# Optimization experiments

Measured on AMD Instinct MI355X. Metric: run time of the kernel, lower is better.

The kernel has to match this reference:

```python
import jax, jax.numpy as jnp
import numpy as np

B, CH, IMG, P = 16, 3, 384, 16
D, HEADS, DH, MLP, DEPTH = 384, 6, 64, 1536, 6
INNER = HEADS * DH
PD = P * P * 5 * CH          # SPT patch dim = 3840
GRID = IMG // P              # 24
NP = GRID * GRID             # 576 patches
SEQ = NP + 1                 # +cls = 577


def layer_norm(x, g, b, eps=1e-5):
    mu = jnp.mean(x, axis=-1, keepdims=True)
    var = jnp.var(x, axis=-1, keepdims=True)
    return (x - mu) * jax.lax.rsqrt(var + eps) * g + b


def spt_shifts(x):
    # F.pad semantics: (left,right,top,bottom) with negative = crop
    s1 = jnp.pad(x, ((0, 0), (0, 0), (0, 0), (1, 0)))[:, :, :, :-1]  # (1,-1,0,0)
    s2 = jnp.pad(x, ((0, 0), (0, 0), (0, 0), (0, 1)))[:, :, :, 1:]   # (-1,1,0,0)
    s3 = jnp.pad(x, ((0, 0), (0, 0), (1, 0), (0, 0)))[:, :, :-1, :]  # (0,0,1,-1)
    s4 = jnp.pad(x, ((0, 0), (0, 0), (0, 1), (0, 0)))[:, :, 1:, :]   # (0,0,-1,1)
    return jnp.concatenate([x, s1, s2, s3, s4], axis=1)  # [b, 5c, H, W]


def patchify(x):
    # 'b c (h p1) (w p2) -> b (h w) (p1 p2 c)'
    b, c, _, _ = x.shape
    x = x.reshape(b, c, GRID, P, GRID, P)
    x = x.transpose(0, 2, 4, 3, 5, 1)  # b h w p1 p2 c
    return x.reshape(b, GRID * GRID, P * P * c)


def setup_inputs():
    key = jax.random.key(0)
    ks = jax.random.split(key, 16)
    img = jax.random.normal(ks[0], (B, CH, IMG, IMG), jnp.float32)
    spt_g = jnp.ones((PD,), jnp.float32)
    spt_b = jnp.zeros((PD,), jnp.float32)
    spt_w = jax.random.normal(ks[1], (PD, D), jnp.float32) * (1.0 / np.sqrt(PD))
    spt_bias = jnp.zeros((D,), jnp.float32)
    pos = jax.random.normal(ks[2], (1, SEQ, D), jnp.float32) * 0.02
    cls = jax.random.normal(ks[3], (1, 1, D), jnp.float32) * 0.02
    attn_g = jnp.ones((DEPTH, D), jnp.float32)
    attn_b = jnp.zeros((DEPTH, D), jnp.float32)
    temp = jnp.full((DEPTH,), np.log(DH ** -0.5), jnp.float32)
    wqkv = jax.random.normal(ks[4], (DEPTH, D, 3 * INNER), jnp.float32) * 0.02
    wout = jax.random.normal(ks[5], (DEPTH, INNER, D), jnp.float32) * 0.02
    bout = jnp.zeros((DEPTH, D), jnp.float32)
    ff_g = jnp.ones((DEPTH, D), jnp.float32)
    ff_b = jnp.zeros((DEPTH, D), jnp.float32)
    w1 = jax.random.normal(ks[6], (DEPTH, D, MLP), jnp.float32) * 0.02
    b1 = jnp.zeros((DEPTH, MLP), jnp.float32)
    w2 = jax.random.normal(ks[7], (DEPTH, MLP, D), jnp.float32) * 0.02
    b2 = jnp.zeros((DEPTH, D), jnp.float32)
    return {"img": img, "spt_g": spt_g, "spt_b": spt_b, "spt_w": spt_w,
            "spt_bias": spt_bias, "pos": pos, "cls": cls, "attn_g": attn_g,
            "attn_b": attn_b, "temp": temp, "wqkv": wqkv, "wout": wout,
            "bout": bout, "ff_g": ff_g, "ff_b": ff_b, "w1": w1, "b1": b1,
            "w2": w2, "b2": b2}


def vit_forward(img, spt_g, spt_b, spt_w, spt_bias, pos, cls, attn_g, attn_b,
                temp, wqkv, wout, bout, ff_g, ff_b, w1, b1, w2, b2):
    # SPT patch embedding
    x = patchify(spt_shifts(img))                      # [b, NP, PD]
    x = layer_norm(x, spt_g, spt_b) @ spt_w + spt_bias  # [b, NP, D]
    b = x.shape[0]
    cls_tok = jnp.broadcast_to(cls, (b, 1, D))
    x = jnp.concatenate([cls_tok, x], axis=1) + pos[:, :SEQ]

    eye = jnp.eye(SEQ, dtype=bool)
    neg = -jnp.finfo(x.dtype).max

    def block(x, p):
        ag, ab, t, wq, wo, bo, fg, fb, W1, B1, W2, B2 = p
        h = layer_norm(x, ag, ab)
        qkv = h @ wq                                   # [b, n, 3*inner]
        q, k, v = jnp.split(qkv, 3, axis=-1)
        q = q.reshape(b, SEQ, HEADS, DH).transpose(0, 2, 1, 3)
        k = k.reshape(b, SEQ, HEADS, DH).transpose(0, 2, 1, 3)
        v = v.reshape(b, SEQ, HEADS, DH).transpose(0, 2, 1, 3)
        dots = jnp.einsum('bhid,bhjd->bhij', q, k) * jnp.exp(t)
        dots = jnp.where(eye, neg, dots)               # diagonal mask (LSA)
        attn = jax.nn.softmax(dots, axis=-1)
        out = jnp.einsum('bhij,bhjd->bhid', attn, v)
        out = out.transpose(0, 2, 1, 3).reshape(b, SEQ, INNER)
        x = out @ wo + bo + x
        h = layer_norm(x, fg, fb)
        x = jax.nn.gelu(h @ W1 + B1, approximate=False) @ W2 + B2 + x
        return x, None

    params = (attn_g, attn_b, temp, wqkv, wout, bout, ff_g, ff_b, w1, b1, w2, b2)
    x, _ = jax.lax.scan(block, x, params)
    return x


def reference(img, spt_g, spt_b, spt_w, spt_bias, pos, cls, attn_g, attn_b,
              temp, wqkv, wout, bout, ff_g, ff_b, w1, b1, w2, b2):
    return vit_forward(img, spt_g, spt_b, spt_w, spt_bias, pos, cls, attn_g,
                       attn_b, temp, wqkv, wout, bout, ff_g, ff_b, w1, b1,
                       w2, b2)
```

## Files before the change

kernel.cpp:

```cpp
#include <hip/hip_runtime.h>

typedef unsigned short ushort_t;
typedef __bf16 bf16x8 __attribute__((ext_vector_type(8)));
typedef float f32x4 __attribute__((ext_vector_type(4)));

#define SEQ_ 577
#define D_ 384
#define NTOK (16 * 577)

enum { M_QKV = 0, M_OUT, M_MLP1, M_MLP2 };

__device__ inline float b2f(ushort_t u) {
    unsigned int x = ((unsigned int)u) << 16;
    float f; __builtin_memcpy(&f, &x, 4); return f;
}
__device__ inline ushort_t f2b(float f) {
    unsigned int x; __builtin_memcpy(&x, &f, 4);
    x = x + 0x7fffu + ((x >> 16) & 1u);
    return (ushort_t)(x >> 16);
}

__device__ void transpose_tile(const float* __restrict__ src,
                               ushort_t* __restrict__ dst,
                               int ldn, int ldk, int k0, int n0)
{
    __shared__ float t[64][65];
    const int tid = threadIdx.x;
    const int c = tid & 63, rr = tid >> 6;
#pragma unroll
    for (int i = 0; i < 16; i++) {
        int kl = rr + i * 4;
        t[kl][c] = src[(size_t)(k0 + kl) * ldn + n0 + c];
    }
    __syncthreads();
#pragma unroll
    for (int i = 0; i < 16; i++) {
        int nl = rr + i * 4;
        dst[(size_t)(n0 + nl) * ldk + k0 + c] = f2b(t[c][nl]);
    }
}

__global__ __launch_bounds__(256) void prep_all_kernel(
    const float* __restrict__ wqkv, const float* __restrict__ wout,
    const float* __restrict__ w1, const float* __restrict__ w2,
    const float* __restrict__ spt_w,
    ushort_t* __restrict__ W6, ushort_t* __restrict__ spt_wt)
{
    int id = blockIdx.x;
    if (id >= 2592) {
        int r2 = id - 2592;
        int kt = r2 % 60, nt = r2 / 60;
        transpose_tile(spt_w, spt_wt, 384, 3840, kt * 64, nt * 64);
        return;
    }
    int l = id / 432;
    int r = id - l * 432;
    ushort_t* qkv_t  = W6 + (size_t)l * 1769472;
    ushort_t* wout_t = qkv_t + 442368;
    ushort_t* w1_t   = wout_t + 147456;
    ushort_t* w2_t   = w1_t + 589824;
    const float* wq = wqkv + (size_t)l * 442368;
    const float* wo = wout + (size_t)l * 147456;
    const float* W1 = w1 + (size_t)l * 589824;
    const float* W2 = w2 + (size_t)l * 589824;
    if (r < 108) {
        int kt = r / 18, nt = r % 18;
        transpose_tile(wq, qkv_t, 1152, 384, kt * 64, nt * 64);
    } else if (r < 144) {
        r -= 108; int kt = r / 6, nt = r % 6;
        transpose_tile(wo, wout_t, 384, 384, kt * 64, nt * 64);
    } else if (r < 288) {
        r -= 144; int kt = r / 24, nt = r % 24;
        transpose_tile(W1, w1_t, 1536, 384, kt * 64, nt * 64);
    } else {
        r -= 288; int kt = r / 6, nt = r % 6;
        transpose_tile(W2, w2_t, 384, 1536, kt * 64, nt * 64);
    }
}

template <int MODE, int NK>
__global__ __launch_bounds__(256) void gemm12864(
    const ushort_t* __restrict__ A, const ushort_t* __restrict__ Bt,
    ushort_t* __restrict__ Co, const float* __restrict__ bias,
    int M, int ldc)
{
    const int K = NK * 32;
    __shared__ __align__(16) ushort_t As[2][128][40];
    __shared__ __align__(16) ushort_t Bs[2][64][40];

    const int gx = gridDim.x;
    const int nwg = gx * gridDim.y;
    const int f = blockIdx.y * gx + blockIdx.x;
    const int q = nwg >> 3, rr_ = nwg & 7;
    const int xcd = f & 7, ii = f >> 3;
    const int swz = (xcd < rr_ ? xcd * (q + 1) : rr_ * (q + 1) + (xcd - rr_) * q) + ii;
    const int bx = swz % gx, by = swz / gx;

    const int tid = threadIdx.x;
    const int rowBase = by * 128;
    const int colBase = bx * 64;
    const int lr = tid >> 2, lk = (tid & 3) * 8;
    const int wv = tid >> 6, lane = tid & 63;
    const int wm = (wv >> 1) * 64, wn = (wv & 1) * 32;
    const int m16 = lane & 15, q4 = lane >> 4, kb = q4 * 8;

    const ushort_t* pa0 = A + (size_t)(rowBase + lr) * K + lk;
    const ushort_t* pa1 = pa0 + (size_t)64 * K;
    const ushort_t* pb  = Bt + (size_t)(colBase + lr) * K + lk;

    f32x4 acc[4][2];
#pragma unroll
    for (int i = 0; i < 4; i++)
#pragma unroll
        for (int j = 0; j < 2; j++) acc[i][j] = (f32x4){0.f, 0.f, 0.f, 0.f};

    uint4 Ua0, Ua1, Ub, Va0, Va1, Vb;
    auto gloadU = [&](int kt) {
        Ua0 = *(const uint4*)(pa0 + kt * 32);
        Ua1 = *(const uint4*)(pa1 + kt * 32);
        Ub  = *(const uint4*)(pb + kt * 32);
    };
    auto gloadV = [&](int kt) {
        Va0 = *(const uint4*)(pa0 + kt * 32);
        Va1 = *(const uint4*)(pa1 + kt * 32);
        Vb  = *(const uint4*)(pb + kt * 32);
    };
    auto swriteU = [&](int buf) {
        *(uint4*)&As[buf][lr][lk] = Ua0;
        *(uint4*)&As[buf][64 + lr][lk] = Ua1;
        *(uint4*)&Bs[buf][lr][lk] = Ub;
    };
    auto swriteV = [&](int buf) {
        *(uint4*)&As[buf][lr][lk] = Va0;
        *(uint4*)&As[buf][64 + lr][lk] = Va1;
        *(uint4*)&Bs[buf][lr][lk] = Vb;
    };
    auto compute = [&](int buf) {
        bf16x8 af[4];
#pragma unroll
        for (int mt = 0; mt < 4; mt++)
            af[mt] = *(const bf16x8*)&As[buf][wm + mt * 16 + m16][kb];
        bf16x8 b0 = *(const bf16x8*)&Bs[buf][wn + m16][kb];
        bf16x8 b1 = *(const bf16x8*)&Bs[buf][wn + 16 + m16][kb];
#pragma unroll
        for (int mt = 0; mt < 4; mt++) {
            acc[mt][0] = __builtin_amdgcn_mfma_f32_16x16x32_bf16(af[mt], b0, acc[mt][0], 0, 0, 0);
            acc[mt][1] = __builtin_amdgcn_mfma_f32_16x16x32_bf16(af[mt], b1, acc[mt][1], 0, 0, 0);
        }
    };

    gloadU(0);
    swriteU(0);
    gloadU(1);
    gloadV(2);
    __syncthreads();

#pragma unroll
    for (int kt = 0; kt < NK; kt += 2) {
        swriteU(1);
        if (kt + 3 < NK) gloadU(kt + 3);
        compute(0);
        __syncthreads();
        if (kt + 2 < NK) {
            swriteV(0);
            if (kt + 4 < NK) gloadV(kt + 4);
        }
        compute(1);
        __syncthreads();
    }

#pragma unroll
    for (int mt = 0; mt < 4; mt++)
#pragma unroll
        for (int nt = 0; nt < 2; nt++) {
            int col = colBase + wn + nt * 16 + m16;
#pragma unroll
            for (int r = 0; r < 4; r++) {
                int row = rowBase + wm + mt * 16 + q4 * 4 + r;
                if (row >= M) continue;
                float v = acc[mt][nt][r];
                if (MODE == M_QKV) {
                    Co[(size_t)row * ldc + col] = f2b(v);
                } else if (MODE == M_MLP1) {
                    float t = v + bias[col];
                    float u = t * (0.7978845608f + 0.0356774081f * t * t);
                    float e = __builtin_amdgcn_exp2f(2.885390082f * u);
                    float gl = t - t * __builtin_amdgcn_rcpf(e + 1.0f);
                    Co[(size_t)row * ldc + col] = f2b(gl);
                }
            }
        }
}

template <int MODE, int NK>
__global__ __launch_bounds__(256) void gemm64(
    const ushort_t* __restrict__ A, const ushort_t* __restrict__ Bt,
    float* __restrict__ resid, const float* __restrict__ bias,
    int M, int ldc)
{
    const int K = NK * 32;
    __shared__ __align__(16) ushort_t As[2][64][40];
    __shared__ __align__(16) ushort_t Bs[2][64][40];

    const int gx = gridDim.x, gy = gridDim.y;
    const int nwg = gx * gy;
    const int f = blockIdx.y * gx + blockIdx.x;
    const int q = nwg >> 3, rr_ = nwg & 7;
    const int xcd = f & 7, ii = f >> 3;
    const int swz = (xcd < rr_ ? xcd * (q + 1) : rr_ * (q + 1) + (xcd - rr_) * q) + ii;
    const int bx = swz % gx, by = swz / gx;

    const int tid = threadIdx.x;
    const int rowBase = by * 64;
    const int colBase = bx * 64;
    const int lr = tid >> 2, lk = (tid & 3) * 8;
    const int wv = tid >> 6, lane = tid & 63;
    const int wm = (wv >> 1) * 32, wn = (wv & 1) * 32;
    const int m16 = lane & 15, q4 = lane >> 4, kb = q4 * 8;

    const ushort_t* pa = A + (size_t)(rowBase + lr) * K + lk;
    const ushort_t* pb = Bt + (size_t)(colBase + lr) * K + lk;

    f32x4 acc[2][2];
#pragma unroll
    for (int i = 0; i < 2; i++)
#pragma unroll
        for (int j = 0; j < 2; j++) acc[i][j] = (f32x4){0.f, 0.f, 0.f, 0.f};

    uint4 Ua, Ub, Va, Vb;
    auto gloadU = [&](int kt) {
        Ua = *(const uint4*)(pa + kt * 32);
        Ub = *(const uint4*)(pb + kt * 32);
    };
    auto gloadV = [&](int kt) {
        Va = *(const uint4*)(pa + kt * 32);
        Vb = *(const uint4*)(pb + kt * 32);
    };
    auto swriteU = [&](int buf) {
        *(uint4*)&As[buf][lr][lk] = Ua;
        *(uint4*)&Bs[buf][lr][lk] = Ub;
    };
    auto swriteV = [&](int buf) {
        *(uint4*)&As[buf][lr][lk] = Va;
        *(uint4*)&Bs[buf][lr][lk] = Vb;
    };
    auto compute = [&](int buf) {
        bf16x8 a0 = *(const bf16x8*)&As[buf][wm + m16][kb];
        bf16x8 a1 = *(const bf16x8*)&As[buf][wm + 16 + m16][kb];
        bf16x8 b0 = *(const bf16x8*)&Bs[buf][wn + m16][kb];
        bf16x8 b1 = *(const bf16x8*)&Bs[buf][wn + 16 + m16][kb];
        acc[0][0] = __builtin_amdgcn_mfma_f32_16x16x32_bf16(a0, b0, acc[0][0], 0, 0, 0);
        acc[0][1] = __builtin_amdgcn_mfma_f32_16x16x32_bf16(a0, b1, acc[0][1], 0, 0, 0);
        acc[1][0] = __builtin_amdgcn_mfma_f32_16x16x32_bf16(a1, b0, acc[1][0], 0, 0, 0);
        acc[1][1] = __builtin_amdgcn_mfma_f32_16x16x32_bf16(a1, b1, acc[1][1], 0, 0, 0);
    };

    gloadU(0);
    swriteU(0);
    gloadU(1);
    gloadV(2);
    __syncthreads();

#pragma unroll
    for (int kt = 0; kt < NK; kt += 2) {
        swriteU(1);
        if (kt + 3 < NK) gloadU(kt + 3);
        compute(0);
        __syncthreads();
        if (kt + 2 < NK) {
            swriteV(0);
            if (kt + 4 < NK) gloadV(kt + 4);
        }
        compute(1);
        __syncthreads();
    }

#pragma unroll
    for (int im = 0; im < 2; im++)
#pragma unroll
        for (int in = 0; in < 2; in++) {
            int col = colBase + wn + in * 16 + m16;
#pragma unroll
            for (int r = 0; r < 4; r++) {
                int row = rowBase + wm + im * 16 + q4 * 4 + r;
                if (row >= M) continue;
                size_t o = (size_t)row * ldc + col;
                resid[o] = resid[o] + acc[im][in][r] + bias[col];
            }
        }
}

__global__ __launch_bounds__(256) void gemm64_spt_split(
    const ushort_t* __restrict__ A, const ushort_t* __restrict__ Bt,
    float* __restrict__ resid, int rowOff)
{
    __shared__ __align__(16) ushort_t As[2][64][40];
    __shared__ __align__(16) ushort_t Bs[2][64][40];

    const int f = blockIdx.z * 288 + blockIdx.y * 6 + blockIdx.x;
    const int swz = (f & 7) * 144 + (f >> 3);
    const int bz = swz / 288;
    const int rem = swz - bz * 288;
    const int by = rem / 6, bx = rem - by * 6;

    const int K = 3840, nk = 30;
    const int rowBase = by * 64;
    const int colBase = bx * 64;
    const int kbase = bz * 960;

    const int tid = threadIdx.x;
    const int lr = tid >> 2, lk = (tid & 3) * 8;
    const int wv = tid >> 6, lane = tid & 63;
    const int wm = (wv >> 1) * 32, wn = (wv & 1) * 32;
    const int m16 = lane & 15, q4 = lane >> 4, kb = q4 * 8;

    const ushort_t* pa = A + (size_t)(rowBase + lr) * K + kbase + lk;
    const ushort_t* pb = Bt + (size_t)(colBase + lr) * K + kbase + lk;

    f32x4 acc[2][2];
#pragma unroll
    for (int i = 0; i < 2; i++)
#pragma unroll
        for (int j = 0; j < 2; j++) acc[i][j] = (f32x4){0.f, 0.f, 0.f, 0.f};

    uint4 Ua, Ub, Va, Vb;
    auto gloadU = [&](int kt) {
        Ua = *(const uint4*)(pa + kt * 32);
        Ub = *(const uint4*)(pb + kt * 32);
    };
    auto gloadV = [&](int kt) {
        Va = *(const uint4*)(pa + kt * 32);
        Vb = *(const uint4*)(pb + kt * 32);
    };
    auto swriteU = [&](int buf) {
        *(uint4*)&As[buf][lr][lk] = Ua;
        *(uint4*)&Bs[buf][lr][lk] = Ub;
    };
    auto swriteV = [&](int buf) {
        *(uint4*)&As[buf][lr][lk] = Va;
        *(uint4*)&Bs[buf][lr][lk] = Vb;
    };
    auto compute = [&](int buf) {
        bf16x8 a0 = *(const bf16x8*)&As[buf][wm + m16][kb];
        bf16x8 a1 = *(const bf16x8*)&As[buf][wm + 16 + m16][kb];
        bf16x8 b0 = *(const bf16x8*)&Bs[buf][wn + m16][kb];
        bf16x8 b1 = *(const bf16x8*)&Bs[buf][wn + 16 + m16][kb];
        acc[0][0] = __builtin_amdgcn_mfma_f32_16x16x32_bf16(a0, b0, acc[0][0], 0, 0, 0);
        acc[0][1] = __builtin_amdgcn_mfma_f32_16x16x32_bf16(a0, b1, acc[0][1], 0, 0, 0);
        acc[1][0] = __builtin_amdgcn_mfma_f32_16x16x32_bf16(a1, b0, acc[1][0], 0, 0, 0);
        acc[1][1] = __builtin_amdgcn_mfma_f32_16x16x32_bf16(a1, b1, acc[1][1], 0, 0, 0);
    };

    gloadU(0);
    swriteU(0);
    gloadU(1);
    gloadV(2);
    __syncthreads();

    for (int kt = 0; kt < nk; kt += 2) {
        swriteU(1);
        if (kt + 3 < nk) gloadU(kt + 3);
        compute(0);
        __syncthreads();
        if (kt + 2 < nk) {
            swriteV(0);
            if (kt + 4 < nk) gloadV(kt + 4);
        }
        compute(1);
        __syncthreads();
    }

#pragma unroll
    for (int im = 0; im < 2; im++)
#pragma unroll
        for (int in = 0; in < 2; in++) {
            int col = colBase + wn + in * 16 + m16;
#pragma unroll
            for (int r = 0; r < 4; r++) {
                int row = rowBase + wm + im * 16 + q4 * 4 + r;
                int grow = rowOff + row;
                int bb = grow / 576, p = grow - bb * 576;
                size_t o = ((size_t)(bb * SEQ_ + 1 + p)) * D_ + col;
                atomicAdd(&resid[o], acc[im][in][r]);
            }
        }
}

__global__ __launch_bounds__(256) void attn_kernel(
    const ushort_t* __restrict__ qkv, ushort_t* __restrict__ attn,
    const float* __restrict__ temp, int layer)
{
    const int f = blockIdx.y * 10 + blockIdx.x;
    const int swz = (f & 7) * 120 + (f >> 3);
    const int qt = swz % 10;
    const int bh = swz / 10;
    const int b = bh / 6, hd = bh - b * 6;
    const int tid = threadIdx.x;
    const int wv = tid >> 6, lane = tid & 63;
    const int m16 = lane & 15, q4 = lane >> 4;
    const float sc2 = expf(temp[layer]) * 1.44269504f;

    __shared__ __align__(16) ushort_t Ks[64][72];
    __shared__ __align__(16) ushort_t Vt[64][72];
    __shared__ __align__(16) ushort_t Pw[4][16][72];

    const int qrow = qt * 64 + wv * 16 + m16;
    const int qtok = qrow < SEQ_ ? qrow : SEQ_ - 1;
    const ushort_t* qb = qkv + ((size_t)(b * SEQ_ + qtok)) * 1152 + hd * 64;
    bf16x8 qf0 = *(const bf16x8*)(qb + q4 * 8);
    bf16x8 qf1 = *(const bf16x8*)(qb + 32 + q4 * 8);

    f32x4 accO[4];
#pragma unroll
    for (int dt = 0; dt < 4; dt++) accO[dt] = (f32x4){0.f, 0.f, 0.f, 0.f};
    float l_r[4] = {0.f, 0.f, 0.f, 0.f};

    const int skey = tid >> 2;
    const int scol = (tid & 3) * 16;
    const int vp   = tid & 31;
    const int vdh  = (tid >> 5) * 8;

    uint4 kv0, kv1, va, vb2;
    auto loadKV = [&](int kt) {
        int key = kt * 64 + skey;
        int gkey = key < SEQ_ ? key : 0;
        const ushort_t* kb_ = qkv + ((size_t)(b * SEQ_ + gkey)) * 1152 + 384 + hd * 64;
        kv0 = *(const uint4*)(kb_ + scol);
        kv1 = *(const uint4*)(kb_ + scol + 8);
        if (key >= SEQ_) { kv0 = (uint4){0, 0, 0, 0}; kv1 = kv0; }
        int vk0 = kt * 64 + 2 * vp;
        int t0 = vk0 < SEQ_ ? vk0 : 0;
        int t1 = vk0 + 1 < SEQ_ ? vk0 + 1 : 0;
        va  = *(const uint4*)(qkv + ((size_t)(b * SEQ_ + t0)) * 1152 + 768 + hd * 64 + vdh);
        vb2 = *(const uint4*)(qkv + ((size_t)(b * SEQ_ + t1)) * 1152 + 768 + hd * 64 + vdh);
        if (vk0 >= SEQ_) va = (uint4){0, 0, 0, 0};
        if (vk0 + 1 >= SEQ_) vb2 = (uint4){0, 0, 0, 0};
    };

    loadKV(0);

    for (int kt = 0; kt < 10; kt++) {
        __syncthreads();
        *(uint4*)&Ks[skey][scol] = kv0;
        *(uint4*)&Ks[skey][scol + 8] = kv1;
        {
            const ushort_t* e0 = (const ushort_t*)&va;
            const ushort_t* e1 = (const ushort_t*)&vb2;
#pragma unroll
            for (int j = 0; j < 8; j++) {
                unsigned int pack = (unsigned int)e0[j] | ((unsigned int)e1[j] << 16);
                *(unsigned int*)&Vt[vdh + j][2 * vp] = pack;
            }
        }
        __syncthreads();
        if (kt + 1 < 10) loadKV(kt + 1);

        f32x4 s[4];
        __builtin_amdgcn_s_setprio(1);
#pragma unroll
        for (int ct = 0; ct < 4; ct++) {
            bf16x8 b0 = *(const bf16x8*)&Ks[ct * 16 + m16][q4 * 8];
            bf16x8 b1 = *(const bf16x8*)&Ks[ct * 16 + m16][32 + q4 * 8];
            f32x4 z = (f32x4){0.f, 0.f, 0.f, 0.f};
            z = __builtin_amdgcn_mfma_f32_16x16x32_bf16(qf0, b0, z, 0, 0, 0);
            z = __builtin_amdgcn_mfma_f32_16x16x32_bf16(qf1, b1, z, 0, 0, 0);
            s[ct] = z;
        }
        __builtin_amdgcn_s_setprio(0);
        const int rowb = qt * 64 + wv * 16 + q4 * 4;
#pragma unroll
        for (int r = 0; r < 4; r++) {
            float rs = 0.f;
#pragma unroll
            for (int ct = 0; ct < 4; ct++) {
                int col = kt * 64 + ct * 16 + m16;
                float v = s[ct][r] * sc2;
                if (col >= SEQ_ || col == rowb + r) v = -1.0e30f;
                float p = __builtin_amdgcn_exp2f(v);
                s[ct][r] = p;
                rs += p;
            }
            rs += __shfl_xor(rs, 1);
            rs += __shfl_xor(rs, 2);
            rs += __shfl_xor(rs, 4);
            rs += __shfl_xor(rs, 8);
            l_r[r] += rs;
        }
#pragma unroll
        for (int ct = 0; ct < 4; ct++)
#pragma unroll
            for (int r = 0; r < 4; r++)
                Pw[wv][q4 * 4 + r][ct * 16 + m16] = f2b(s[ct][r]);
        bf16x8 pf0 = *(const bf16x8*)&Pw[wv][m16][q4 * 8];
        bf16x8 pf1 = *(const bf16x8*)&Pw[wv][m16][32 + q4 * 8];
        __builtin_amdgcn_s_setprio(1);
#pragma unroll
        for (int dt = 0; dt < 4; dt++) {
            bf16x8 vb0 = *(const bf16x8*)&Vt[dt * 16 + m16][q4 * 8];
            bf16x8 vb1 = *(const bf16x8*)&Vt[dt * 16 + m16][32 + q4 * 8];
            f32x4 o = accO[dt];
            o = __builtin_amdgcn_mfma_f32_16x16x32_bf16(pf0, vb0, o, 0, 0, 0);
            o = __builtin_amdgcn_mfma_f32_16x16x32_bf16(pf1, vb1, o, 0, 0, 0);
            accO[dt] = o;
        }
        __builtin_amdgcn_s_setprio(0);
    }

    const int rowb = qt * 64 + wv * 16 + q4 * 4;
#pragma unroll
    for (int r = 0; r < 4; r++) {
        int grow = rowb + r;
        if (grow >= SEQ_) continue;
        float inv = 1.f / l_r[r];
        ushort_t* op = attn + ((size_t)(b * SEQ_ + grow)) * 384 + hd * 64;
#pragma unroll
        for (int dt = 0; dt < 4; dt++)
            op[dt * 16 + m16] = f2b(accO[dt][r] * inv);
    }
}

__global__ __launch_bounds__(256) void spt_ln_kernel(
    const float* __restrict__ img, const float* __restrict__ gg,
    const float* __restrict__ bb_, ushort_t* __restrict__ Xn, int r0)
{
    int bp = r0 + blockIdx.x;
    int b = bp / 576, p = bp - b * 576;
    int ph = p / 24, pw = p - ph * 24;

    __shared__ float vals[3840];
    __shared__ float red[10];

    const int tid = threadIdx.x;
    const int p1 = tid >> 4, p2 = tid & 15;

    float s = 0.f, sq = 0.f;
#pragma unroll
    for (int plane = 0; plane < 15; plane++) {
        int g5 = plane / 3, ch = plane - g5 * 3;
        int row = ph * 16 + p1, col = pw * 16 + p2;
        if (g5 == 1) col -= 1;
        else if (g5 == 2) col += 1;
        else if (g5 == 3) row -= 1;
        else if (g5 == 4) row += 1;
        float v = 0.f;
        if (row >= 0 && row < 384 && col >= 0 && col < 384)
            v = img[((size_t)(b * 3 + ch) * 384 + row) * 384 + col];
        vals[tid * 15 + plane] = v;
        s += v; sq += v * v;
    }
#pragma unroll
    for (int off = 32; off > 0; off >>= 1) {
        s += __shfl_xor(s, off);
        sq += __shfl_xor(sq, off);
    }
    int wid = tid >> 6;
    if ((tid & 63) == 0) { red[wid] = s; red[4 + wid] = sq; }
    __syncthreads();
    if (tid == 0) {
        float S = red[0] + red[1] + red[2] + red[3];
        float Q = red[4] + red[5] + red[6] + red[7];
        float mean = S / 3840.f;
        float var = Q / 3840.f - mean * mean;
        red[8] = mean;
        red[9] = rsqrtf(var + 1e-5f);
    }
    __syncthreads();
    float mean = red[8], rstd = red[9];
#pragma unroll
    for (int i = 0; i < 15; i++) {
        int k = tid + i * 256;
        float v = (vals[k] - mean) * rstd * gg[k] + bb_[k];
        Xn[(size_t)blockIdx.x * 3840 + k] = f2b(v);
    }
}

__global__ __launch_bounds__(256) void ln_kernel(
    const float* __restrict__ x, const float* __restrict__ g,
    const float* __restrict__ b, ushort_t* __restrict__ h)
{
    int row = blockIdx.x * 4 + (threadIdx.x >> 6);
    int lane = threadIdx.x & 63;
    const float* xr = x + (size_t)row * 384;
    float4 a = *(const float4*)(xr + lane * 4);
    float2 c = *(const float2*)(xr + 256 + lane * 2);
    float s = a.x + a.y + a.z + a.w + c.x + c.y;
    float sq = a.x * a.x + a.y * a.y + a.z * a.z + a.w * a.w
             + c.x * c.x + c.y * c.y;
#pragma unroll
    for (int off = 32; off > 0; off >>= 1) {
        s += __shfl_xor(s, off);
        sq += __shfl_xor(sq, off);
    }
    float mean = s / 384.f;
    float var = sq / 384.f - mean * mean;
    float rstd = rsqrtf(var + 1e-5f);
    float4 gv = *(const float4*)(g + lane * 4);
    float2 gc = *(const float2*)(g + 256 + lane * 2);
    float4 bv = *(const float4*)(b + lane * 4);
    float2 bc = *(const float2*)(b + 256 + lane * 2);
    ushort_t* hr = h + (size_t)row * 384;
    {
        unsigned int lo = (unsigned int)f2b((a.x - mean) * rstd * gv.x + bv.x)
                        | ((unsigned int)f2b((a.y - mean) * rstd * gv.y + bv.y) << 16);
        unsigned int hi = (unsigned int)f2b((a.z - mean) * rstd * gv.z + bv.z)
                        | ((unsigned int)f2b((a.w - mean) * rstd * gv.w + bv.w) << 16);
        *(uint2*)&hr[lane * 4] = make_uint2(lo, hi);
    }
    {
        unsigned int w = (unsigned int)f2b((c.x - mean) * rstd * gc.x + bc.x)
                       | ((unsigned int)f2b((c.y - mean) * rstd * gc.y + bc.y) << 16);
        *(unsigned int*)&hr[256 + lane * 2] = w;
    }
}

__global__ void init_x_kernel(const float* __restrict__ cls,
                              const float* __restrict__ pos,
                              const float* __restrict__ spt_bias,
                              float* __restrict__ x)
{
    int s = blockIdx.x, b = blockIdx.y, d = threadIdx.x;
    float base = (s == 0) ? cls[d] : spt_bias[d];
    x[((size_t)b * SEQ_ + s) * D_ + d] = base + pos[(size_t)s * D_ + d];
}

extern "C" void kernel_launch(void* const* d_in, const int* in_sizes, int n_in,
                              void* d_out, int out_size, void* d_ws, size_t ws_size,
                              hipStream_t stream)
{
    const float* img      = (const float*)d_in[0];
    const float* spt_g    = (const float*)d_in[1];
    const float* spt_b    = (const float*)d_in[2];
    const float* spt_w    = (const float*)d_in[3];
    const float* spt_bias = (const float*)d_in[4];
    const float* pos      = (const float*)d_in[5];
    const float* clsp     = (const float*)d_in[6];
    const float* attn_g   = (const float*)d_in[7];
    const float* attn_b   = (const float*)d_in[8];
    const float* temp     = (const float*)d_in[9];
    const float* wqkv     = (const float*)d_in[10];
    const float* wout     = (const float*)d_in[11];
    const float* bout     = (const float*)d_in[12];
    const float* ff_g     = (const float*)d_in[13];
    const float* ff_b     = (const float*)d_in[14];
    const float* w1       = (const float*)d_in[15];
    const float* b1       = (const float*)d_in[16];
    const float* w2       = (const float*)d_in[17];
    const float* b2       = (const float*)d_in[18];

    float* x = (float*)d_out;

    char* base = (char*)d_ws;
    ushort_t* qkv   = (ushort_t*)base;
    ushort_t* attn  = (ushort_t*)(base + (size_t)NTOK * 1152 * 2);
    ushort_t* Xn    = (ushort_t*)base;
    ushort_t* gbuf  = (ushort_t*)base;
    ushort_t* spt_wt = (ushort_t*)(base + 23592960);
    char* p2 = base + (size_t)NTOK * 1536 * 2;
    ushort_t* h  = (ushort_t*)p2;
    char* p3 = p2 + (size_t)NTOK * 384 * 2;
    ushort_t* W6 = (ushort_t*)p3;

    prep_all_kernel<<<2952, 256, 0, stream>>>(wqkv, wout, w1, w2, spt_w, W6, spt_wt);
    init_x_kernel<<<dim3(SEQ_, 16), 384, 0, stream>>>(clsp, pos, spt_bias, x);

    for (int c = 0; c < 3; c++) {
        int r0 = c * 3072;
        spt_ln_kernel<<<3072, 256, 0, stream>>>(img, spt_g, spt_b, Xn, r0);
        gemm64_spt_split<<<dim3(6, 48, 4), 256, 0, stream>>>(Xn, spt_wt, x, r0);
    }

    for (int l = 0; l < 6; l++) {
        ushort_t* qkv_t  = W6 + (size_t)l * 1769472;
        ushort_t* wout_t = qkv_t + 442368;
        ushort_t* w1_t   = wout_t + 147456;
        ushort_t* w2_t   = w1_t + 589824;
        ln_kernel<<<NTOK / 4, 256, 0, stream>>>(x, attn_g + l * 384, attn_b + l * 384, h);
        gemm12864<M_QKV, 12><<<dim3(18, 73), 256, 0, stream>>>(
            h, qkv_t, qkv, nullptr, NTOK, 1152);
        attn_kernel<<<dim3(10, 96), 256, 0, stream>>>(qkv, attn, temp, l);
        gemm64<M_OUT, 12><<<dim3(6, 145), 256, 0, stream>>>(
            attn, wout_t, x, bout + l * 384, NTOK, 384);
        ln_kernel<<<NTOK / 4, 256, 0, stream>>>(x, ff_g + l * 384, ff_b + l * 384, h);
        gemm12864<M_MLP1, 12><<<dim3(24, 73), 256, 0, stream>>>(
            h, w1_t, gbuf, b1 + l * 1536, NTOK, 1536);
        gemm64<M_MLP2, 48><<<dim3(6, 145), 256, 0, stream>>>(
            gbuf, w2_t, x, b2 + l * 384, NTOK, 384);
    }
}
```

Before: 1.113 ms.

## Fuse FF layernorm into MLP1 GEMM via row stats from out-proj epilogue

The out-projection GEMM epilogue now computes per-row partial sums and sums of squares and writes them to a stats buffer. A new MLP1 GEMM variant reads the fp32 residual directly, rebuilds mean and rstd from those partials, and normalizes and converts to bf16 while staging A tiles into shared memory. This removes the separate ln_kernel launch and the bf16 h round trip. In exchange, the MLP1 kernel loads twice as many A bytes (fp32 instead of bf16), each of its 24 column blocks repeats the normalization, and variance is computed as E[x²]−mean², which is less numerically stable.

Result: slower. 1.236 ms (+11.1%).

```diff
diff --git a/kernel.cpp b/kernel.cpp
--- a/kernel.cpp
+++ b/kernel.cpp
@@ -192,11 +192,165 @@
         }
 }
 
+template <int NK>
+__global__ __launch_bounds__(256) void gemm12864_ln(
+    const float* __restrict__ X, const ushort_t* __restrict__ Bt,
+    ushort_t* __restrict__ Co, const float* __restrict__ bias,
+    const float* __restrict__ stats, const float* __restrict__ lng,
+    const float* __restrict__ lnb, int M, int ldc)
+{
+    const int K = NK * 32;
+    __shared__ __align__(16) ushort_t As[2][128][40];
+    __shared__ __align__(16) ushort_t Bs[2][64][40];
+
+    const int gx = gridDim.x;
+    const int nwg = gx * gridDim.y;
+    const int f = blockIdx.y * gx + blockIdx.x;
+    const int q = nwg >> 3, rr_ = nwg & 7;
+    const int xcd = f & 7, ii = f >> 3;
+    const int swz = (xcd < rr_ ? xcd * (q + 1) : rr_ * (q + 1) + (xcd - rr_) * q) + ii;
+    const int bx = swz % gx, by = swz / gx;
+
+    const int tid = threadIdx.x;
+    const int rowBase = by * 128;
+    const int colBase = bx * 64;
+    const int lr = tid >> 2, lk = (tid & 3) * 8;
+    const int wv = tid >> 6, lane = tid & 63;
+    const int wm = (wv >> 1) * 64, wn = (wv & 1) * 32;
+    const int m16 = lane & 15, q4 = lane >> 4, kb = q4 * 8;
+
+    int ar0 = rowBase + lr;       if (ar0 >= M) ar0 = M - 1;
+    int ar1 = rowBase + 64 + lr;  if (ar1 >= M) ar1 = M - 1;
+
+    float rstd0, nc0, rstd1, nc1;
+    {
+        const float4* sp = (const float4*)(stats + (size_t)ar0 * 24);
+        float s = 0.f, sq = 0.f;
+#pragma unroll
+        for (int i = 0; i < 6; i++) { float4 v = sp[i]; s += v.x + v.z; sq += v.y + v.w; }
+        float mean = s * (1.f / 384.f);
+        rstd0 = rsqrtf(sq * (1.f / 384.f) - mean * mean + 1e-5f);
+        nc0 = -mean * rstd0;
+    }
+    {
+        const float4* sp = (const float4*)(stats + (size_t)ar1 * 24);
+        float s = 0.f, sq = 0.f;
+#pragma unroll
+        for (int i = 0; i < 6; i++) { float4 v = sp[i]; s += v.x + v.z; sq += v.y + v.w; }
+        float mean = s * (1.f / 384.f);
+        rstd1 = rsqrtf(sq * (1.f / 384.f) - mean * mean + 1e-5f);
+        nc1 = -mean * rstd1;
+    }
+
+    const float* px0 = X + (size_t)ar0 * K + lk;
+    const float* px1 = X + (size_t)ar1 * K + lk;
+    const ushort_t* pb = Bt + (size_t)(colBase + lr) * K + lk;
+
+    f32x4 acc[4][2];
+#pragma unroll
+    for (int i = 0; i < 4; i++)
+#pragma unroll
+        for (int j = 0; j < 2; j++) acc[i][j] = (f32x4){0.f, 0.f, 0.f, 0.f};
+
+    float4 U0a, U0b, U1a, U1b, V0a, V0b, V1a, V1b;
+    uint4 Ub, Vb;
+    auto gloadU = [&](int kt) {
+        const float4* p0 = (const float4*)(px0 + kt * 32);
+        U0a = p0[0]; U0b = p0[1];
+        const float4* p1 = (const float4*)(px1 + kt * 32);
+        U1a = p1[0]; U1b = p1[1];
+        Ub = *(const uint4*)(pb + kt * 32);
+    };
+    auto gloadV = [&](int kt) {
+        const float4* p0 = (const float4*)(px0 + kt * 32);
+        V0a = p0[0]; V0b = p0[1];
+        const float4* p1 = (const float4*)(px1 + kt * 32);
+        V1a = p1[0]; V1b = p1[1];
+        Vb = *(const uint4*)(pb + kt * 32);
+    };
+    auto nrm8 = [&](float4 a, float4 b2, float rstd, float nc, int ktd) -> bf16x8 {
+        const float4 g0 = *(const float4*)(lng + ktd * 32 + lk);
+        const float4 g1 = *(const float4*)(lng + ktd * 32 + lk + 4);
+        const float4 bb0 = *(const float4*)(lnb + ktd * 32 + lk);
+        const float4 bb1 = *(const float4*)(lnb + ktd * 32 + lk + 4);
+        bf16x8 r;
+        r[0] = (__bf16)(fmaf(a.x, rstd, nc) * g0.x + bb0.x);
+        r[1] = (__bf16)(fmaf(a.y, rstd, nc) * g0.y + bb0.y);
+        r[2] = (__bf16)(fmaf(a.z, rstd, nc) * g0.z + bb0.z);
+        r[3] = (__bf16)(fmaf(a.w, rstd, nc) * g0.w + bb0.w);
+        r[4] = (__bf16)(fmaf(b2.x, rstd, nc) * g1.x + bb1.x);
+        r[5] = (__bf16)(fmaf(b2.y, rstd, nc) * g1.y + bb1.y);
+        r[6] = (__bf16)(fmaf(b2.z, rstd, nc) * g1.z + bb1.z);
+        r[7] = (__bf16)(fmaf(b2.w, rstd, nc) * g1.w + bb1.w);
+        return r;
+    };
+    auto swriteU = [&](int buf, int ktd) {
+        *(bf16x8*)&As[buf][lr][lk] = nrm8(U0a, U0b, rstd0, nc0, ktd);
+        *(bf16x8*)&As[buf][64 + lr][lk] = nrm8(U1a, U1b, rstd1, nc1, ktd);
+        *(uint4*)&Bs[buf][lr][lk] = Ub;
+    };
+    auto swriteV = [&](int buf, int ktd) {
+        *(bf16x8*)&As[buf][lr][lk] = nrm8(V0a, V0b, rstd0, nc0, ktd);
+        *(bf16x8*)&As[buf][64 + lr][lk] = nrm8(V1a, V1b, rstd1, nc1, ktd);
+        *(uint4*)&Bs[buf][lr][lk] = Vb;
+    };
+    auto compute = [&](int buf) {
+        bf16x8 af[4];
+#pragma unroll
+        for (int mt = 0; mt < 4; mt++)
+            af[mt] = *(const bf16x8*)&As[buf][wm + mt * 16 + m16][kb];
+        bf16x8 b0 = *(const bf16x8*)&Bs[buf][wn + m16][kb];
+        bf16x8 b1 = *(const bf16x8*)&Bs[buf][wn + 16 + m16][kb];
+#pragma unroll
+        for (int mt = 0; mt < 4; mt++) {
+            acc[mt][0] = __builtin_amdgcn_mfma_f32_16x16x32_bf16(af[mt], b0, acc[mt][0], 0, 0, 0);
+            acc[mt][1] = __builtin_amdgcn_mfma_f32_16x16x32_bf16(af[mt], b1, acc[mt][1], 0, 0, 0);
+        }
+    };
+
+    gloadU(0);
+    swriteU(0, 0);
+    gloadU(1);
+    gloadV(2);
+    __syncthreads();
+
+#pragma unroll
+    for (int kt = 0; kt < NK; kt += 2) {
+        swriteU(1, kt + 1);
+        if (kt + 3 < NK) gloadU(kt + 3);
+        compute(0);
+        __syncthreads();
+        if (kt + 2 < NK) {
+            swriteV(0, kt + 2);
+            if (kt + 4 < NK) gloadV(kt + 4);
+        }
+        compute(1);
+        __syncthreads();
+    }
+
+#pragma unroll
+    for (int mt = 0; mt < 4; mt++)
+#pragma unroll
+        for (int nt = 0; nt < 2; nt++) {
+            int col = colBase + wn + nt * 16 + m16;
+#pragma unroll
+            for (int r = 0; r < 4; r++) {
+                int row = rowBase + wm + mt * 16 + q4 * 4 + r;
+                if (row >= M) continue;
+                float t = acc[mt][nt][r] + bias[col];
+                float u = t * (0.7978845608f + 0.0356774081f * t * t);
+                float e = __builtin_amdgcn_exp2f(2.885390082f * u);
+                float gl = t - t * __builtin_amdgcn_rcpf(e + 1.0f);
+                Co[(size_t)row * ldc + col] = f2b(gl);
+            }
+        }
+}
+
 template <int MODE, int NK>
 __global__ __launch_bounds__(256) void gemm64(
     const ushort_t* __restrict__ A, const ushort_t* __restrict__ Bt,
     float* __restrict__ resid, const float* __restrict__ bias,
-    int M, int ldc)
+    float* __restrict__ stats, int M, int ldc)
 {
     const int K = NK * 32;
     __shared__ __align__(16) ushort_t As[2][64][40];
@@ -278,14 +432,29 @@
 #pragma unroll
     for (int im = 0; im < 2; im++)
 #pragma unroll
-        for (int in = 0; in < 2; in++) {
-            int col = colBase + wn + in * 16 + m16;
-#pragma unroll
-            for (int r = 0; r < 4; r++) {
-                int row = rowBase + wm + im * 16 + q4 * 4 + r;
-                if (row >= M) continue;
-                size_t o = (size_t)row * ldc + col;
-                resid[o] = resid[o] + acc[im][in][r] + bias[col];
+        for (int r = 0; r < 4; r++) {
+            int row = rowBase + wm + im * 16 + q4 * 4 + r;
+            float s = 0.f, sq = 0.f;
+#pragma unroll
+            for (int in = 0; in < 2; in++) {
+                int col = colBase + wn + in * 16 + m16;
+                if (row < M) {
+                    size_t o = (size_t)row * ldc + col;
+                    float v = resid[o] + acc[im][in][r] + bias[col];
+                    resid[o] = v;
+                    s += v; sq += v * v;
+                }
+            }
+            if (MODE == M_OUT) {
+                s += __shfl_xor(s, 1);  s += __shfl_xor(s, 2);
+                s += __shfl_xor(s, 4);  s += __shfl_xor(s, 8);
+                sq += __shfl_xor(sq, 1); sq += __shfl_xor(sq, 2);
+                sq += __shfl_xor(sq, 4); sq += __shfl_xor(sq, 8);
+                if (m16 == 0 && row < M) {
+                    int slot = bx * 2 + (wv & 1);
+                    stats[(size_t)row * 24 + slot * 2]     = s;
+                    stats[(size_t)row * 24 + slot * 2 + 1] = sq;
+                }
             }
         }
 }
@@ -657,6 +826,7 @@
     ushort_t* spt_wt = (ushort_t*)(base + 23592960);
     char* p2 = base + (size_t)NTOK * 1536 * 2;
     ushort_t* h  = (ushort_t*)p2;
+    float* stats = (float*)p2;
     char* p3 = p2 + (size_t)NTOK * 384 * 2;
     ushort_t* W6 = (ushort_t*)p3;
 
@@ -679,11 +849,11 @@
             h, qkv_t, qkv, nullptr, NTOK, 1152);
         attn_kernel<<<dim3(10, 96), 256, 0, stream>>>(qkv, attn, temp, l);
         gemm64<M_OUT, 12><<<dim3(6, 145), 256, 0, stream>>>(
-            attn, wout_t, x, bout + l * 384, NTOK, 384);
-        ln_kernel<<<NTOK / 4, 256, 0, stream>>>(x, ff_g + l * 384, ff_b + l * 384, h);
-        gemm12864<M_MLP1, 12><<<dim3(24, 73), 256, 0, stream>>>(
-            h, w1_t, gbuf, b1 + l * 1536, NTOK, 1536);
+            attn, wout_t, x, bout + l * 384, stats, NTOK, 384);
+        gemm12864_ln<12><<<dim3(24, 73), 256, 0, stream>>>(
+            x, w1_t, gbuf, b1 + l * 1536, stats, ff_g + l * 384, ff_b + l * 384,
+            NTOK, 1536);
         gemm64<M_MLP2, 48><<<dim3(6, 145), 256, 0, stream>>>(
-            gbuf, w2_t, x, b2 + l * 384, NTOK, 384);
-    }
-}
+            gbuf, w2_t, x, b2 + l * 384, nullptr, NTOK, 384);
+    }
+}
```
